# Optimization experiments

Measured on AMD Instinct MI355X. Metric: run time of the kernel, lower is better.

Reference implementation:

```python
import jax, jax.numpy as jnp
import numpy as np

B, NQ, NM, NHR, D, H, FF = 16, 100, 5440, 4096, 256, 8, 2048

def _ln(x, w, b):
    m = x.mean(-1, keepdims=True)
    v = ((x - m) ** 2).mean(-1, keepdims=True)
    return (x - m) * jax.lax.rsqrt(v + 1e-5) * w + b

def setup_inputs():
    key = jax.random.key(0)
    ks = iter(jax.random.split(key, 32))
    def rn(shape, s=1.0):
        return jax.random.normal(next(ks), shape, jnp.float32) * s
    return {
        'tgt': rn((B, NQ, D)),
        'memory': rn((B, NM, D)),
        'memory_hr': rn((B, NHR, D)),
        'prior_attn_bias': rn((B, NQ, NM)),
        'query_pos': rn((B, NQ, D)),
        'ln_cross_w': jnp.ones((D,)), 'ln_cross_b': jnp.zeros((D,)),
        'q_w': rn((D, D), 0.02), 'q_b': jnp.zeros((D,)),
        'k_w': rn((D, D), 0.02), 'k_b': jnp.zeros((D,)),
        'v_w': rn((D, D), 0.02), 'v_b': jnp.zeros((D,)),
        'out_w': rn((D, D), 0.02), 'out_b': jnp.zeros((D,)),
        'ln_self_w': jnp.ones((D,)), 'ln_self_b': jnp.zeros((D,)),
        'sa_in_w': rn((3 * D, D), 0.02), 'sa_in_b': jnp.zeros((3 * D,)),
        'sa_out_w': rn((D, D), 0.02), 'sa_out_b': jnp.zeros((D,)),
        'ln_ffn_w': jnp.ones((D,)), 'ln_ffn_b': jnp.zeros((D,)),
        'lin1_w': rn((FF, D), 0.02), 'lin1_b': jnp.zeros((FF,)),
        'lin2_w': rn((D, FF), 0.02), 'lin2_b': jnp.zeros((D,)),
        'me_w': rn((D, D), 0.02), 'me_b': jnp.zeros((D,)),
    }

def reference(tgt, memory, memory_hr, prior_attn_bias, query_pos,
              ln_cross_w, ln_cross_b, q_w, q_b, k_w, k_b, v_w, v_b,
              out_w, out_b, ln_self_w, ln_self_b, sa_in_w, sa_in_b,
              sa_out_w, sa_out_b, ln_ffn_w, ln_ffn_b, lin1_w, lin1_b,
              lin2_w, lin2_b, me_w, me_b):
    b, nq, d = tgt.shape
    nm = memory.shape[1]
    h = H
    dh = d // h
    scale = dh ** -0.5
    # ---- cross-attention with additive prior bias (eval mode: dropout = id) ----
    x = _ln(tgt, ln_cross_w, ln_cross_b)
    q = ((x + query_pos) @ q_w.T + q_b).reshape(b, nq, h, dh)
    k = (memory @ k_w.T + k_b).reshape(b, nm, h, dh)
    v = (memory @ v_w.T + v_b).reshape(b, nm, h, dh)
    attn = jnp.einsum('bqhd,bmhd->bhqm', q, k) * scale + prior_attn_bias[:, None]  # [b,h,nq,nm]
    a = jax.nn.softmax(attn, axis=-1)
    o = jnp.einsum('bhqm,bmhd->bqhd', a, v).reshape(b, nq, d)
    tgt = tgt + (o @ out_w.T + out_b)
    # ---- self-attention (torch nn.MultiheadAttention, batch_first, eval) ----
    z = _ln(tgt, ln_self_w, ln_self_b)
    zq = z + query_pos
    qs = (zq @ sa_in_w[:d].T + sa_in_b[:d]).reshape(b, nq, h, dh)
    ks = (zq @ sa_in_w[d:2 * d].T + sa_in_b[d:2 * d]).reshape(b, nq, h, dh)
    vs = (z @ sa_in_w[2 * d:].T + sa_in_b[2 * d:]).reshape(b, nq, h, dh)
    sattn = jax.nn.softmax(jnp.einsum('bqhd,bmhd->bhqm', qs, ks) * scale, axis=-1)
    so = jnp.einsum('bhqm,bmhd->bqhd', sattn, vs).reshape(b, nq, d)
    tgt = tgt + (so @ sa_out_w.T + sa_out_b)
    # ---- FFN ----
    y = _ln(tgt, ln_ffn_w, ln_ffn_b)
    y = jax.nn.gelu(y @ lin1_w.T + lin1_b, approximate=False) @ lin2_w.T + lin2_b
    tgt = tgt + y
    # ---- mask branch ----
    mask_logits = jnp.einsum('bqd,bmd->bqm', tgt @ me_w.T + me_b, memory_hr)
    return (tgt, mask_logits)
```

## Files before the change

kernel.cpp:

```cpp
#include <hip/hip_runtime.h>

typedef unsigned short u16;
typedef unsigned int u32;
typedef __bf16 bf16x8 __attribute__((ext_vector_type(8)));
typedef float f32x4 __attribute__((ext_vector_type(4)));

__device__ __forceinline__ u16 f2b(float f) {
  u32 u = __float_as_uint(f);
  u32 r = (u + 0x7fffu + ((u >> 16) & 1u)) >> 16;
  return (u16)r;
}
__device__ __forceinline__ float b2f(u16 h) {
  return __uint_as_float(((u32)h) << 16);
}
__device__ __forceinline__ bf16x8 zero8() {
  union { uint4 u; bf16x8 v; } z; z.u = make_uint4(0u, 0u, 0u, 0u); return z.v;
}
__device__ __forceinline__ u32 cvtpk(float lo, float hi) {
  u32 r;
  asm("v_cvt_pk_bf16_f32 %0, %1, %2" : "=v"(r) : "v"(lo), "v"(hi));
  return r;
}

struct Seg { const float* in; u16* out; int n4; };
struct Segs { Seg s[9]; };

__global__ __launch_bounds__(256)
void f2b_multi_kernel(Segs segs) {
  const Seg sg = segs.s[blockIdx.y];
  const int i = blockIdx.x * 256 + threadIdx.x;
  if (i < sg.n4) {
    const float4 f = *(const float4*)(sg.in + (size_t)i * 4);
    uint2 pk;
    pk.x = (u32)f2b(f.x) | ((u32)f2b(f.y) << 16);
    pk.y = (u32)f2b(f.z) | ((u32)f2b(f.w) << 16);
    *(uint2*)(sg.out + (size_t)i * 4) = pk;
  }
}

__global__ void copy_bias_kernel(const float* __restrict__ a, const float* __restrict__ b,
                                 float* __restrict__ out) {
  int i = threadIdx.x;
  out[i] = (i < 256) ? a[i] : b[i - 256];
}

__global__ __launch_bounds__(256)
void bias_tr_kernel(const float* __restrict__ bias, u16* __restrict__ biasT)
{
  __shared__ float S[100][69];
  const int tid = threadIdx.x;
  const int m0 = blockIdx.x * 64, b = blockIdx.y;
  for (int idx = tid; idx < 1600; idx += 256) {
    const int q = idx >> 4, seg = idx & 15;
    const float4 v = *(const float4*)(bias + (size_t)(b * 100 + q) * 5440 + m0 + seg * 4);
    S[q][seg * 4 + 0] = v.x; S[q][seg * 4 + 1] = v.y;
    S[q][seg * 4 + 2] = v.z; S[q][seg * 4 + 3] = v.w;
  }
  __syncthreads();
  for (int idx = tid; idx < 1792; idx += 256) {
    const int m = idx / 28, qg = (idx % 28) * 4;
    u16 h[4];
#pragma unroll
    for (int r = 0; r < 4; ++r) {
      const int q = qg + r;
      h[r] = (q < 100) ? f2b(S[q][m]) : (u16)0;
    }
    uint2 pk;
    pk.x = (u32)h[0] | ((u32)h[1] << 16);
    pk.y = (u32)h[2] | ((u32)h[3] << 16);
    *(uint2*)(biasT + ((size_t)(b * 5440 + m0 + m)) * 112 + qg) = pk;
  }
}

__global__ __launch_bounds__(256)
void ln_kernel(const float* __restrict__ x, const float* __restrict__ w, const float* __restrict__ b,
               const float* __restrict__ pos, u16* __restrict__ outz, u16* __restrict__ outzq)
{
  const int lane = threadIdx.x & 63;
  const int row = blockIdx.x * 4 + (threadIdx.x >> 6);
  const size_t o = (size_t)row * 256 + lane * 4;
  const float4 v = *(const float4*)(x + o);
  float s = v.x + v.y + v.z + v.w;
#pragma unroll
  for (int m = 1; m < 64; m <<= 1) s += __shfl_xor(s, m);
  const float mean = s * (1.f / 256.f);
  const float d0 = v.x - mean, d1 = v.y - mean, d2 = v.z - mean, d3 = v.w - mean;
  float ss = d0 * d0 + d1 * d1 + d2 * d2 + d3 * d3;
#pragma unroll
  for (int m = 1; m < 64; m <<= 1) ss += __shfl_xor(ss, m);
  const float rs = rsqrtf(ss * (1.f / 256.f) + 1e-5f);
  const float4 wv = *(const float4*)(w + lane * 4);
  const float4 bv = *(const float4*)(b + lane * 4);
  float y0 = d0 * rs * wv.x + bv.x;
  float y1 = d1 * rs * wv.y + bv.y;
  float y2 = d2 * rs * wv.z + bv.z;
  float y3 = d3 * rs * wv.w + bv.w;
  if (outz) {
    uint2 pk;
    pk.x = (u32)f2b(y0) | ((u32)f2b(y1) << 16);
    pk.y = (u32)f2b(y2) | ((u32)f2b(y3) << 16);
    *(uint2*)(outz + o) = pk;
  }
  if (outzq) {
    const float4 pv = *(const float4*)(pos + o);
    uint2 pk;
    pk.x = (u32)f2b(y0 + pv.x) | ((u32)f2b(y1 + pv.y) << 16);
    pk.y = (u32)f2b(y2 + pv.z) | ((u32)f2b(y3 + pv.w) << 16);
    *(uint2*)(outzq + o) = pk;
  }
}

template<int BM, int BN, int WM, int WN, int AF32, int GELU_, int RES_, int OF32, int OBF>
__global__ __launch_bounds__(256)
void gemm_kernel(const void* __restrict__ Ap, const u16* __restrict__ W,
                 const float* __restrict__ bias, const float* __restrict__ res,
                 float* __restrict__ Cf, u16* __restrict__ Cb,
                 int M, int N, int K, float scale)
{
  constexpr int WROWS = BM / WM;
  constexpr int WCOLS = BN / WN;
  constexpr int MT = WROWS / 16;
  constexpr int NT = WCOLS / 16;
  static_assert(WM * WN == 4, "4 waves");
  __shared__ u16 As[BM][40];
  __shared__ u16 Ws[BN][40];
  const int tid = threadIdx.x, lane = tid & 63, wid = tid >> 6;
  const int g = lane >> 4, lr = lane & 15;
  const int m0 = blockIdx.x * BM, n0 = blockIdx.y * BN;
  const int wm = wid / WN, wn = wid % WN;
  f32x4 acc[MT][NT] = {};
  for (int k0 = 0; k0 < K; k0 += 32) {
    for (int cid = tid; cid < BM * 4; cid += 256) {
      int r = cid >> 2, cg = (cid & 3) * 8;
      if constexpr (AF32) {
        const float* ap = (const float*)Ap + (size_t)(m0 + r) * K + k0 + cg;
        float4 f0 = *(const float4*)ap;
        float4 f1 = *(const float4*)(ap + 4);
        uint4 pk;
        pk.x = (u32)f2b(f0.x) | ((u32)f2b(f0.y) << 16);
        pk.y = (u32)f2b(f0.z) | ((u32)f2b(f0.w) << 16);
        pk.z = (u32)f2b(f1.x) | ((u32)f2b(f1.y) << 16);
        pk.w = (u32)f2b(f1.z) | ((u32)f2b(f1.w) << 16);
        *(uint4*)&As[r][cg] = pk;
      } else {
        *(uint4*)&As[r][cg] = *(const uint4*)((const u16*)Ap + (size_t)(m0 + r) * K + k0 + cg);
      }
    }
    for (int cid = tid; cid < BN * 4; cid += 256) {
      int r = cid >> 2, cg = (cid & 3) * 8;
      *(uint4*)&Ws[r][cg] = *(const uint4*)(W + (size_t)(n0 + r) * K + k0 + cg);
    }
    __syncthreads();
    bf16x8 af[MT], bfr[NT];
#pragma unroll
    for (int mt = 0; mt < MT; ++mt) af[mt] = *(const bf16x8*)&As[wm * WROWS + mt * 16 + lr][g * 8];
#pragma unroll
    for (int nt = 0; nt < NT; ++nt) bfr[nt] = *(const bf16x8*)&Ws[wn * WCOLS + nt * 16 + lr][g * 8];
#pragma unroll
    for (int mt = 0; mt < MT; ++mt)
#pragma unroll
      for (int nt = 0; nt < NT; ++nt)
        acc[mt][nt] = __builtin_amdgcn_mfma_f32_16x16x32_bf16(af[mt], bfr[nt], acc[mt][nt], 0, 0, 0);
    __syncthreads();
  }
#pragma unroll
  for (int mt = 0; mt < MT; ++mt)
#pragma unroll
    for (int nt = 0; nt < NT; ++nt) {
      const int col = n0 + wn * WCOLS + nt * 16 + lr;
      const float bv = bias[col];
#pragma unroll
      for (int r = 0; r < 4; ++r) {
        const int row = m0 + wm * WROWS + mt * 16 + g * 4 + r;
        float v = (acc[mt][nt][r] + bv) * scale;
        if constexpr (GELU_) v = 0.5f * v * (1.f + erff(v * 0.70710678118654752f));
        if constexpr (RES_) v += res[(size_t)row * N + col];
        if constexpr (OF32) Cf[(size_t)row * N + col] = v;
        if constexpr (OBF) Cb[(size_t)row * N + col] = f2b(v);
      }
    }
}

__global__ __launch_bounds__(512, 4)
void kv_gemm_kernel(const float* __restrict__ A, const u16* __restrict__ Wk,
                    const u16* __restrict__ Wv, const float* __restrict__ biasKV,
                    u16* __restrict__ Kb, u16* __restrict__ Vt)
{
  __shared__ u16 As[64 * 256];
  const int tid = threadIdx.x, lane = tid & 63, wid = tid >> 6;
  const int g = lane >> 4, lr = lane & 15;
  const int bidx = blockIdx.x / 85, t = blockIdx.x - bidx * 85;
  const int row0 = blockIdx.x * 64;

  for (int ch = tid; ch < 2048; ch += 512) {
    const int r = ch >> 5, c8 = (ch & 31) * 8;
    const float* ap = A + (size_t)(row0 + r) * 256 + c8;
    const float4 f0 = *(const float4*)ap;
    const float4 f1 = *(const float4*)(ap + 4);
    uint4 pk;
    pk.x = cvtpk(f0.x, f0.y);
    pk.y = cvtpk(f0.z, f0.w);
    pk.z = cvtpk(f1.x, f1.y);
    pk.w = cvtpk(f1.z, f1.w);
    const int byte = r * 512 + c8 * 2;
    *(uint4*)((char*)As + (byte ^ ((r & 7) << 4))) = pk;
  }
  __syncthreads();

  const int isV = wid >> 2;
  const u16* W = isV ? Wv : Wk;
  const int n0 = (wid & 3) * 64;
  const u16* Wb[4];
#pragma unroll
  for (int nt = 0; nt < 4; ++nt)
    Wb[nt] = W + (size_t)(n0 + nt * 16 + lr) * 256 + g * 8;

  f32x4 acc[4][4] = {};
#pragma unroll 2
  for (int ks = 0; ks < 8; ++ks) {
    bf16x8 bfv[4], af[4];
#pragma unroll
    for (int nt = 0; nt < 4; ++nt)
      bfv[nt] = *(const bf16x8*)(Wb[nt] + ks * 32);
#pragma unroll
    for (int mt = 0; mt < 4; ++mt) {
      const int r = mt * 16 + lr;
      const int byte = r * 512 + ks * 64 + g * 16;
      af[mt] = *(const bf16x8*)((const char*)As + (byte ^ ((r & 7) << 4)));
    }
#pragma unroll
    for (int mt = 0; mt < 4; ++mt)
#pragma unroll
      for (int nt = 0; nt < 4; ++nt)
        acc[mt][nt] = __builtin_amdgcn_mfma_f32_16x16x32_bf16(af[mt], bfv[nt], acc[mt][nt], 0, 0, 0);
  }

  if (!isV) {
#pragma unroll
    for (int nt = 0; nt < 4; ++nt) {
      const int col = n0 + nt * 16 + lr;
      const float bv = biasKV[col];
#pragma unroll
      for (int mt = 0; mt < 4; ++mt)
#pragma unroll
        for (int r = 0; r < 4; ++r)
          Kb[(size_t)(row0 + mt * 16 + g * 4 + r) * 256 + col] = f2b(acc[mt][nt][r] + bv);
    }
  } else {
    const int mloc0 = t * 64;
#pragma unroll
    for (int nt = 0; nt < 4; ++nt) {
      const int col = n0 + nt * 16 + lr;
      const float bv = biasKV[256 + col];
      const size_t rowbase = ((size_t)(bidx * 8 + (col >> 5)) * 32 + (col & 31)) * 5440;
#pragma unroll
      for (int mt = 0; mt < 4; ++mt)
#pragma unroll
        for (int r = 0; r < 4; ++r) {
          const int mloc = mloc0 + mt * 16 + g * 4 + r;
          const int ml = mloc & 31;
          const int p = 8 * ((ml & 15) >> 2) + 2 * (ml & 3) + (ml >> 4);
          Vt[rowbase + (mloc & ~31) + p] = f2b(acc[mt][nt][r] + bv);
        }
    }
  }
}

__global__ __launch_bounds__(256, 3)
void cross_attn_kernel(const u16* __restrict__ Q, const u16* __restrict__ Kb,
                       const u16* __restrict__ Vt, const u16* __restrict__ biasT,
                       float* __restrict__ Opart, float* __restrict__ ML)
{
  __shared__ u32 P32[4][112][20];
  const int tid = threadIdx.x, lane = tid & 63, wid = tid >> 6;
  const int g = lane >> 4, lr = lane & 15;
  const int b = blockIdx.y, c = blockIdx.x;
  const int head = blockIdx.z * 4 + wid;
  const int m_base = c * 320;
  const f32x4 zf = {0.f, 0.f, 0.f, 0.f};

  bf16x8 qf[7];
#pragma unroll
  for (int mt = 0; mt < 7; ++mt) {
    int qr = mt * 16 + lr;
    qf[mt] = (qr < 100) ? *(const bf16x8*)&Q[(size_t)(b * 100 + qr) * 256 + head * 32 + g * 8]
                        : zero8();
  }
  float Mst[7];
  f32x4 Lp[7];
  f32x4 Oa[7][2];
#pragma unroll
  for (int mt = 0; mt < 7; ++mt) { Mst[mt] = -1e30f; Lp[mt] = zf; Oa[mt][0] = zf; Oa[mt][1] = zf; }

  for (int s = 0; s < 10; ++s) {
    const int m0 = m_base + s * 32;
    const bf16x8 kf0 = *(const bf16x8*)&Kb[(size_t)(b * 5440 + m0 + lr) * 256 + head * 32 + g * 8];
    const bf16x8 kf1 = *(const bf16x8*)&Kb[(size_t)(b * 5440 + m0 + 16 + lr) * 256 + head * 32 + g * 8];
    const size_t vrow = ((size_t)(b * 8 + head) * 32 + lr) * 5440 + m0 + g * 8;
    const bf16x8 vf0 = *(const bf16x8*)&Vt[vrow];
    const bf16x8 vf1 = *(const bf16x8*)&Vt[vrow + 16 * 5440];
    const u16* bb = biasT + ((size_t)(b * 5440 + m0 + lr)) * 112 + g * 4;
#pragma unroll
    for (int mt = 0; mt < 7; ++mt) {
      f32x4 s0 = __builtin_amdgcn_mfma_f32_16x16x32_bf16(qf[mt], kf0, zf, 0, 0, 0);
      f32x4 s1 = __builtin_amdgcn_mfma_f32_16x16x32_bf16(qf[mt], kf1, zf, 0, 0, 0);
      const uint2 b0 = *(const uint2*)(bb + mt * 16);
      const uint2 b1 = *(const uint2*)(bb + 16 * 112 + mt * 16);
      s0[0] += b2f((u16)b0.x);      s0[1] += b2f((u16)(b0.x >> 16));
      s0[2] += b2f((u16)b0.y);      s0[3] += b2f((u16)(b0.y >> 16));
      s1[0] += b2f((u16)b1.x);      s1[1] += b2f((u16)(b1.x >> 16));
      s1[2] += b2f((u16)b1.y);      s1[3] += b2f((u16)(b1.y >> 16));
      float mx = fmaxf(fmaxf(fmaxf(s0[0], s0[1]), fmaxf(s0[2], s0[3])),
                       fmaxf(fmaxf(s1[0], s1[1]), fmaxf(s1[2], s1[3])));
#pragma unroll
      for (int d = 1; d < 16; d <<= 1) mx = fmaxf(mx, __shfl_xor(mx, d, 16));
      const float newM = fmaxf(Mst[mt], mx);
      const float al = __expf(Mst[mt] - newM);
      Mst[mt] = newM;
      f32x4 p0, p1;
#pragma unroll
      for (int r = 0; r < 4; ++r) {
        p0[r] = __expf(s0[r] - newM);
        p1[r] = __expf(s1[r] - newM);
      }
      Lp[mt] = Lp[mt] * al + (p0 + p1);
      Oa[mt][0] *= al;
      Oa[mt][1] *= al;
#pragma unroll
      for (int r = 0; r < 4; ++r)
        P32[wid][mt * 16 + g * 4 + r][lr] = (u32)f2b(p0[r]) | ((u32)f2b(p1[r]) << 16);
    }
#pragma unroll
    for (int mt = 0; mt < 7; ++mt) {
      const bf16x8 pa = *(const bf16x8*)&P32[wid][mt * 16 + lr][g * 4];
      Oa[mt][0] = __builtin_amdgcn_mfma_f32_16x16x32_bf16(pa, vf0, Oa[mt][0], 0, 0, 0);
      Oa[mt][1] = __builtin_amdgcn_mfma_f32_16x16x32_bf16(pa, vf1, Oa[mt][1], 0, 0, 0);
    }
  }
  const int bh = b * 8 + head;
#pragma unroll
  for (int mt = 0; mt < 7; ++mt)
#pragma unroll
    for (int r = 0; r < 4; ++r) {
      const int qr = mt * 16 + g * 4 + r;
      if (qr < 100) {
        float L = Lp[mt][r];
#pragma unroll
        for (int d = 1; d < 16; d <<= 1) L += __shfl_xor(L, d, 16);
        const size_t rb = (size_t)(bh * 17 + c) * 100 + qr;
        Opart[rb * 32 + lr] = Oa[mt][0][r];
        Opart[rb * 32 + 16 + lr] = Oa[mt][1][r];
        if (lr == 0) { ML[rb * 2] = Mst[mt]; ML[rb * 2 + 1] = L; }
      }
    }
}

__global__ __launch_bounds__(256)
void reduce_attn_kernel(const float* __restrict__ Opart, const float* __restrict__ ML,
                        u16* __restrict__ outb)
{
  const int row = blockIdx.x;
  const int b = row / 100, q = row % 100;
  const int h = threadIdx.x >> 5, d = threadIdx.x & 31;
  const int bh = b * 8 + h;
  float gm = -1e30f;
  for (int c = 0; c < 17; ++c) gm = fmaxf(gm, ML[((size_t)(bh * 17 + c) * 100 + q) * 2]);
  float l = 0.f, o = 0.f;
  for (int c = 0; c < 17; ++c) {
    const size_t rb = (size_t)(bh * 17 + c) * 100 + q;
    const float w = __expf(ML[rb * 2] - gm);
    l += ML[rb * 2 + 1] * w;
    o += Opart[rb * 32 + d] * w;
  }
  outb[(size_t)row * 256 + h * 32 + d] = f2b(o / l);
}

__global__ __launch_bounds__(128)
void self_attn_kernel(const float* __restrict__ qk, const float* __restrict__ vs,
                      u16* __restrict__ so)
{
  __shared__ u16 kk[100][36];
  __shared__ u16 vv[100][36];
  __shared__ float S[100][101];
  const int b = blockIdx.x >> 3, h = blockIdx.x & 7;
  const int t = threadIdx.x;
  for (int e = t; e < 3200; e += 128) {
    const int r = e >> 5, cq = e & 31;
    kk[r][cq] = f2b(qk[(size_t)(b * 100 + r) * 512 + 256 + h * 32 + cq]);
    vv[r][cq] = f2b(vs[(size_t)(b * 100 + r) * 256 + h * 32 + cq]);
  }
  __syncthreads();
  if (t < 100) {
    float qr_[32];
#pragma unroll
    for (int cq = 0; cq < 32; ++cq) qr_[cq] = qk[(size_t)(b * 100 + t) * 512 + h * 32 + cq];
    for (int m = 0; m < 100; ++m) {
      float dp = 0.f;
#pragma unroll
      for (int cq = 0; cq < 32; ++cq) dp += qr_[cq] * b2f(kk[m][cq]);
      S[t][m] = dp * 0.17677669529663687f;
    }
    float mx = -1e30f;
    for (int m = 0; m < 100; ++m) mx = fmaxf(mx, S[t][m]);
    float sum = 0.f;
    for (int m = 0; m < 100; ++m) { const float p = __expf(S[t][m] - mx); S[t][m] = p; sum += p; }
    const float inv = 1.f / sum;
    float o[32];
#pragma unroll
    for (int cq = 0; cq < 32; ++cq) o[cq] = 0.f;
    for (int m = 0; m < 100; ++m) {
      const float p = S[t][m];
#pragma unroll
      for (int cq = 0; cq < 32; ++cq) o[cq] += p * b2f(vv[m][cq]);
    }
#pragma unroll
    for (int cq = 0; cq < 32; ++cq)
      so[(size_t)(b * 100 + t) * 256 + h * 32 + cq] = f2b(o[cq] * inv);
  }
}

__global__ __launch_bounds__(256)
void mask_gemm_kernel(const u16* __restrict__ tm, const float* __restrict__ hr,
                      float* __restrict__ out)
{
  __shared__ u16 As[112][40];
  __shared__ u16 Bs[64][40];
  const int tid = threadIdx.x, lane = tid & 63, wid = tid >> 6;
  const int g = lane >> 4, lr = lane & 15;
  const int b = blockIdx.y, n0 = blockIdx.x * 64;
  f32x4 acc[7] = {};
  for (int k0 = 0; k0 < 256; k0 += 32) {
    for (int cid = tid; cid < 448; cid += 256) {
      const int r = cid >> 2, cg = (cid & 3) * 8;
      uint4 val = {0u, 0u, 0u, 0u};
      if (r < 100) val = *(const uint4*)&tm[(size_t)(b * 100 + r) * 256 + k0 + cg];
      *(uint4*)&As[r][cg] = val;
    }
    {
      const int r = tid >> 2, cg = (tid & 3) * 8;
      const float* hp = hr + (size_t)(b * 4096 + n0 + r) * 256 + k0 + cg;
      float4 f0 = *(const float4*)hp;
      float4 f1 = *(const float4*)(hp + 4);
      uint4 pk;
      pk.x = (u32)f2b(f0.x) | ((u32)f2b(f0.y) << 16);
      pk.y = (u32)f2b(f0.z) | ((u32)f2b(f0.w) << 16);
      pk.z = (u32)f2b(f1.x) | ((u32)f2b(f1.y) << 16);
      pk.w = (u32)f2b(f1.z) | ((u32)f2b(f1.w) << 16);
      *(uint4*)&Bs[r][cg] = pk;
    }
    __syncthreads();
    const bf16x8 bfr = *(const bf16x8*)&Bs[wid * 16 + lr][g * 8];
#pragma unroll
    for (int mt = 0; mt < 7; ++mt) {
      const bf16x8 af = *(const bf16x8*)&As[mt * 16 + lr][g * 8];
      acc[mt] = __builtin_amdgcn_mfma_f32_16x16x32_bf16(af, bfr, acc[mt], 0, 0, 0);
    }
    __syncthreads();
  }
#pragma unroll
  for (int mt = 0; mt < 7; ++mt)
#pragma unroll
    for (int r = 0; r < 4; ++r) {
      const int qr = mt * 16 + g * 4 + r;
      if (qr < 100)
        out[(size_t)(b * 100 + qr) * 4096 + n0 + wid * 16 + lr] = acc[mt][r];
    }
}

extern "C" void kernel_launch(void* const* d_in, const int* in_sizes, int n_in,
                              void* d_out, int out_size, void* d_ws, size_t ws_size,
                              hipStream_t stream)
{
  (void)in_sizes; (void)n_in; (void)out_size; (void)ws_size;
  const float* tgt      = (const float*)d_in[0];
  const float* memory   = (const float*)d_in[1];
  const float* memhr    = (const float*)d_in[2];
  const float* pbias    = (const float*)d_in[3];
  const float* qpos     = (const float*)d_in[4];
  const float* lncw     = (const float*)d_in[5];
  const float* lncb     = (const float*)d_in[6];
  const float* q_w      = (const float*)d_in[7];
  const float* q_b      = (const float*)d_in[8];
  const float* k_w      = (const float*)d_in[9];
  const float* k_b      = (const float*)d_in[10];
  const float* v_w      = (const float*)d_in[11];
  const float* v_b      = (const float*)d_in[12];
  const float* out_w    = (const float*)d_in[13];
  const float* out_b    = (const float*)d_in[14];
  const float* lnsw     = (const float*)d_in[15];
  const float* lnsb     = (const float*)d_in[16];
  const float* sa_in_w  = (const float*)d_in[17];
  const float* sa_in_b  = (const float*)d_in[18];
  const float* sa_out_w = (const float*)d_in[19];
  const float* sa_out_b = (const float*)d_in[20];
  const float* lnfw     = (const float*)d_in[21];
  const float* lnfb     = (const float*)d_in[22];
  const float* l1w      = (const float*)d_in[23];
  const float* l1b      = (const float*)d_in[24];
  const float* l2w      = (const float*)d_in[25];
  const float* l2b      = (const float*)d_in[26];
  const float* me_w     = (const float*)d_in[27];
  const float* me_b     = (const float*)d_in[28];
  float* outf = (float*)d_out;

  char* ws = (char*)d_ws;
  size_t off = 0;
  auto alloc = [&](size_t bytes) -> void* {
    void* p = ws + off;
    off = (off + bytes + 255) & ~(size_t)255;
    return p;
  };
  u16*   kvW   = (u16*)alloc((size_t)131072 * 2);
  u16*   qW    = (u16*)alloc((size_t)65536 * 2);
  u16*   outW  = (u16*)alloc((size_t)65536 * 2);
  u16*   saW   = (u16*)alloc((size_t)196608 * 2);
  u16*   saoW  = (u16*)alloc((size_t)65536 * 2);
  u16*   l1W   = (u16*)alloc((size_t)524288 * 2);
  u16*   l2W   = (u16*)alloc((size_t)524288 * 2);
  u16*   meW   = (u16*)alloc((size_t)65536 * 2);
  float* kvB   = (float*)alloc((size_t)512 * 4);
  u16*   biasT = (u16*)alloc((size_t)9748480 * 2);
  u16*   zq1   = (u16*)alloc((size_t)409600 * 2);
  u16*   Qb    = (u16*)alloc((size_t)409600 * 2);
  u16*   Kb    = (u16*)alloc((size_t)22282240 * 2);
  u16*   Vt    = (u16*)alloc((size_t)22282240 * 2);
  float* Opart = (float*)alloc((size_t)6963200 * 4);
  float* MLp   = (float*)alloc((size_t)435200 * 4);
  u16*   attno = (u16*)alloc((size_t)409600 * 2);
  float* tgt1  = (float*)alloc((size_t)409600 * 4);
  u16*   z2    = (u16*)alloc((size_t)409600 * 2);
  u16*   zq2   = (u16*)alloc((size_t)409600 * 2);
  float* qkb   = (float*)alloc((size_t)819200 * 4);
  float* vsb   = (float*)alloc((size_t)409600 * 4);
  u16*   sob   = (u16*)alloc((size_t)409600 * 2);
  float* tgt2  = (float*)alloc((size_t)409600 * 4);
  u16*   y0b   = (u16*)alloc((size_t)409600 * 2);
  u16*   hb    = (u16*)alloc((size_t)3276800 * 2);
  u16*   t3b   = (u16*)alloc((size_t)409600 * 2);
  u16*   tmb   = (u16*)alloc((size_t)409600 * 2);

  const float SCALE = 0.17677669529663687f;

  Segs segs;
  segs.s[0] = {k_w,      kvW,          16384};
  segs.s[1] = {v_w,      kvW + 65536,  16384};
  segs.s[2] = {q_w,      qW,           16384};
  segs.s[3] = {out_w,    outW,         16384};
  segs.s[4] = {sa_in_w,  saW,          49152};
  segs.s[5] = {sa_out_w, saoW,         16384};
  segs.s[6] = {l1w,      l1W,          131072};
  segs.s[7] = {l2w,      l2W,          131072};
  segs.s[8] = {me_w,     meW,          16384};
  f2b_multi_kernel<<<dim3(512, 9), 256, 0, stream>>>(segs);
  copy_bias_kernel<<<1, 512, 0, stream>>>(k_b, v_b, kvB);
  bias_tr_kernel<<<dim3(85, 16), 256, 0, stream>>>(pbias, biasT);

  ln_kernel<<<400, 256, 0, stream>>>(tgt, lncw, lncb, qpos, nullptr, zq1);
  gemm_kernel<16, 128, 1, 4, 0, 0, 0, 0, 1><<<dim3(100, 2), 256, 0, stream>>>(
      zq1, qW, q_b, nullptr, nullptr, Qb, 1600, 256, 256, SCALE);
  kv_gemm_kernel<<<dim3(1360), 512, 0, stream>>>(memory, kvW, kvW + 65536, kvB, Kb, Vt);
  cross_attn_kernel<<<dim3(17, 16, 2), 256, 0, stream>>>(Qb, Kb, Vt, biasT, Opart, MLp);
  reduce_attn_kernel<<<1600, 256, 0, stream>>>(Opart, MLp, attno);
  gemm_kernel<16, 128, 1, 4, 0, 0, 1, 1, 0><<<dim3(100, 2), 256, 0, stream>>>(
      attno, outW, out_b, tgt, tgt1, nullptr, 1600, 256, 256, 1.f);

  ln_kernel<<<400, 256, 0, stream>>>(tgt1, lnsw, lnsb, qpos, z2, zq2);
  gemm_kernel<16, 128, 1, 4, 0, 0, 0, 1, 0><<<dim3(100, 4), 256, 0, stream>>>(
      zq2, saW, sa_in_b, nullptr, qkb, nullptr, 1600, 512, 256, 1.f);
  gemm_kernel<16, 128, 1, 4, 0, 0, 0, 1, 0><<<dim3(100, 2), 256, 0, stream>>>(
      z2, saW + 131072, sa_in_b + 512, nullptr, vsb, nullptr, 1600, 256, 256, 1.f);
  self_attn_kernel<<<128, 128, 0, stream>>>(qkb, vsb, sob);
  gemm_kernel<16, 128, 1, 4, 0, 0, 1, 1, 0><<<dim3(100, 2), 256, 0, stream>>>(
      sob, saoW, sa_out_b, tgt1, tgt2, nullptr, 1600, 256, 256, 1.f);

  ln_kernel<<<400, 256, 0, stream>>>(tgt2, lnfw, lnfb, nullptr, y0b, nullptr);
  gemm_kernel<64, 256, 4, 1, 0, 1, 0, 0, 1><<<dim3(25, 8), 256, 0, stream>>>(
      y0b, l1W, l1b, nullptr, nullptr, hb, 1600, 2048, 256, 1.f);
  gemm_kernel<16, 128, 1, 4, 0, 0, 1, 1, 1><<<dim3(100, 2), 256, 0, stream>>>(
      hb, l2W, l2b, tgt2, outf, t3b, 1600, 256, 2048, 1.f);

  gemm_kernel<16, 128, 1, 4, 0, 0, 0, 0, 1><<<dim3(100, 2), 256, 0, stream>>>(
      t3b, meW, me_b, nullptr, nullptr, tmb, 1600, 256, 256, 1.f);
  mask_gemm_kernel<<<dim3(64, 16), 256, 0, stream>>>(tmb, memhr, outf + 409600);
}
```

Baseline: 370.7 us.

## Fuse prep kernels, fold layernorms into GEMMs, restage KV epilogue via LDS

```diff
diff --git a/kernel.cpp b/kernel.cpp
--- a/kernel.cpp
+++ b/kernel.cpp
@@ -23,96 +23,231 @@
 }
 
 struct Seg { const float* in; u16* out; int n4; };
-struct Segs { Seg s[9]; };
+struct PrepArgs {
+  Seg seg[7];
+  const float *k_w, *v_w, *k_b, *v_b, *pbias;
+  u16 *Wf, *biasT;
+  float *kvB;
+};
 
 __global__ __launch_bounds__(256)
-void f2b_multi_kernel(Segs segs) {
-  const Seg sg = segs.s[blockIdx.y];
-  const int i = blockIdx.x * 256 + threadIdx.x;
-  if (i < sg.n4) {
-    const float4 f = *(const float4*)(sg.in + (size_t)i * 4);
-    uint2 pk;
-    pk.x = (u32)f2b(f.x) | ((u32)f2b(f.y) << 16);
-    pk.y = (u32)f2b(f.z) | ((u32)f2b(f.w) << 16);
-    *(uint2*)(sg.out + (size_t)i * 4) = pk;
-  }
-}
-
-__global__ void copy_bias_kernel(const float* __restrict__ a, const float* __restrict__ b,
-                                 float* __restrict__ out) {
-  int i = threadIdx.x;
-  out[i] = (i < 256) ? a[i] : b[i - 256];
-}
-
-__global__ __launch_bounds__(256)
-void bias_tr_kernel(const float* __restrict__ bias, u16* __restrict__ biasT)
+void prep_kernel(PrepArgs a)
 {
   __shared__ float S[100][69];
-  const int tid = threadIdx.x;
-  const int m0 = blockIdx.x * 64, b = blockIdx.y;
-  for (int idx = tid; idx < 1600; idx += 256) {
-    const int q = idx >> 4, seg = idx & 15;
-    const float4 v = *(const float4*)(bias + (size_t)(b * 100 + q) * 5440 + m0 + seg * 4);
-    S[q][seg * 4 + 0] = v.x; S[q][seg * 4 + 1] = v.y;
-    S[q][seg * 4 + 2] = v.z; S[q][seg * 4 + 3] = v.w;
-  }
-  __syncthreads();
-  for (int idx = tid; idx < 1792; idx += 256) {
-    const int m = idx / 28, qg = (idx % 28) * 4;
-    u16 h[4];
-#pragma unroll
-    for (int r = 0; r < 4; ++r) {
-      const int q = qg + r;
-      h[r] = (q < 100) ? f2b(S[q][m]) : (u16)0;
-    }
-    uint2 pk;
-    pk.x = (u32)h[0] | ((u32)h[1] << 16);
-    pk.y = (u32)h[2] | ((u32)h[3] << 16);
-    *(uint2*)(biasT + ((size_t)(b * 5440 + m0 + m)) * 112 + qg) = pk;
-  }
-}
-
-__global__ __launch_bounds__(256)
-void ln_kernel(const float* __restrict__ x, const float* __restrict__ w, const float* __restrict__ b,
-               const float* __restrict__ pos, u16* __restrict__ outz, u16* __restrict__ outzq)
-{
-  const int lane = threadIdx.x & 63;
-  const int row = blockIdx.x * 4 + (threadIdx.x >> 6);
-  const size_t o = (size_t)row * 256 + lane * 4;
-  const float4 v = *(const float4*)(x + o);
-  float s = v.x + v.y + v.z + v.w;
-#pragma unroll
-  for (int m = 1; m < 64; m <<= 1) s += __shfl_xor(s, m);
-  const float mean = s * (1.f / 256.f);
-  const float d0 = v.x - mean, d1 = v.y - mean, d2 = v.z - mean, d3 = v.w - mean;
-  float ss = d0 * d0 + d1 * d1 + d2 * d2 + d3 * d3;
-#pragma unroll
-  for (int m = 1; m < 64; m <<= 1) ss += __shfl_xor(ss, m);
-  const float rs = rsqrtf(ss * (1.f / 256.f) + 1e-5f);
+  const int bx = blockIdx.x, tid = threadIdx.x;
+  if (bx < 1472) {
+    int bxr = bx;
+#pragma unroll
+    for (int k = 0; k < 7; ++k) {
+      const int nb = a.seg[k].n4 >> 8;
+      if (bxr < nb) {
+        const int i = bxr * 256 + tid;
+        const float4 f = *(const float4*)(a.seg[k].in + (size_t)i * 4);
+        uint2 pk; pk.x = cvtpk(f.x, f.y); pk.y = cvtpk(f.z, f.w);
+        *(uint2*)(a.seg[k].out + (size_t)i * 4) = pk;
+        return;
+      }
+      bxr -= nb;
+    }
+    return;
+  } else if (bx < 1536) {
+    const int i = bx - 1472, gI = i >> 3, ks = i & 7;
+    const int nt = tid >> 6, lane = tid & 63, lr = lane & 15, g = lane >> 4;
+    const float* src = (gI < 4 ? a.k_w + (size_t)(gI * 64 + nt * 16 + lr) * 256
+                               : a.v_w + (size_t)((gI - 4) * 64 + nt * 16 + lr) * 256)
+                       + ks * 32 + g * 8;
+    const float4 f0 = *(const float4*)src;
+    const float4 f1 = *(const float4*)(src + 4);
+    uint4 pk;
+    pk.x = cvtpk(f0.x, f0.y); pk.y = cvtpk(f0.z, f0.w);
+    pk.z = cvtpk(f1.x, f1.y); pk.w = cvtpk(f1.z, f1.w);
+    *(uint4*)(a.Wf + (size_t)((gI * 8 + ks) * 4 + nt) * 512 + lane * 8) = pk;
+  } else if (bx < 1538) {
+    const int i = (bx - 1536) * 256 + tid;
+    a.kvB[i] = (i < 256) ? a.k_b[i] : a.v_b[i - 256];
+  } else {
+    const int bt = bx - 1538;
+    const int b = bt / 85, m0 = (bt - b * 85) * 64;
+    for (int idx = tid; idx < 1600; idx += 256) {
+      const int q = idx >> 4, seg = idx & 15;
+      const float4 v = *(const float4*)(a.pbias + (size_t)(b * 100 + q) * 5440 + m0 + seg * 4);
+      S[q][seg * 4 + 0] = v.x; S[q][seg * 4 + 1] = v.y;
+      S[q][seg * 4 + 2] = v.z; S[q][seg * 4 + 3] = v.w;
+    }
+    __syncthreads();
+    for (int idx = tid; idx < 1792; idx += 256) {
+      const int m = idx / 28, qg = (idx % 28) * 4;
+      u16 h[4];
+#pragma unroll
+      for (int r = 0; r < 4; ++r) {
+        const int q = qg + r;
+        h[r] = (q < 100) ? f2b(S[q][m]) : (u16)0;
+      }
+      uint2 pk;
+      pk.x = (u32)h[0] | ((u32)h[1] << 16);
+      pk.y = (u32)h[2] | ((u32)h[3] << 16);
+      *(uint2*)(a.biasT + ((size_t)(b * 5440 + m0 + m)) * 112 + qg) = pk;
+    }
+  }
+}
+
+template<int ROWS>
+__device__ __forceinline__ void ln_stage(const float* __restrict__ x, int row0,
+    const float* __restrict__ w, const float* __restrict__ b,
+    const float* __restrict__ pos, u16* As)
+{
+  const int tid = threadIdx.x, lane = tid & 63, wid = tid >> 6;
   const float4 wv = *(const float4*)(w + lane * 4);
   const float4 bv = *(const float4*)(b + lane * 4);
-  float y0 = d0 * rs * wv.x + bv.x;
-  float y1 = d1 * rs * wv.y + bv.y;
-  float y2 = d2 * rs * wv.z + bv.z;
-  float y3 = d3 * rs * wv.w + bv.w;
-  if (outz) {
-    uint2 pk;
-    pk.x = (u32)f2b(y0) | ((u32)f2b(y1) << 16);
-    pk.y = (u32)f2b(y2) | ((u32)f2b(y3) << 16);
-    *(uint2*)(outz + o) = pk;
-  }
-  if (outzq) {
-    const float4 pv = *(const float4*)(pos + o);
-    uint2 pk;
-    pk.x = (u32)f2b(y0 + pv.x) | ((u32)f2b(y1 + pv.y) << 16);
-    pk.y = (u32)f2b(y2 + pv.z) | ((u32)f2b(y3 + pv.w) << 16);
-    *(uint2*)(outzq + o) = pk;
-  }
-}
-
-template<int BM, int BN, int WM, int WN, int AF32, int GELU_, int RES_, int OF32, int OBF>
+#pragma unroll
+  for (int rr = 0; rr < ROWS / 4; ++rr) {
+    const int rl = wid * (ROWS / 4) + rr;
+    const size_t o = (size_t)(row0 + rl) * 256 + lane * 4;
+    const float4 v = *(const float4*)(x + o);
+    float s = v.x + v.y + v.z + v.w;
+#pragma unroll
+    for (int m = 1; m < 64; m <<= 1) s += __shfl_xor(s, m);
+    const float mean = s * (1.f / 256.f);
+    const float d0 = v.x - mean, d1 = v.y - mean, d2 = v.z - mean, d3 = v.w - mean;
+    float ss = d0 * d0 + d1 * d1 + d2 * d2 + d3 * d3;
+#pragma unroll
+    for (int m = 1; m < 64; m <<= 1) ss += __shfl_xor(ss, m);
+    const float rs = rsqrtf(ss * (1.f / 256.f) + 1e-5f);
+    float y0 = d0 * rs * wv.x + bv.x;
+    float y1 = d1 * rs * wv.y + bv.y;
+    float y2 = d2 * rs * wv.z + bv.z;
+    float y3 = d3 * rs * wv.w + bv.w;
+    if (pos) {
+      const float4 pv = *(const float4*)(pos + o);
+      y0 += pv.x; y1 += pv.y; y2 += pv.z; y3 += pv.w;
+    }
+    uint2 pk; pk.x = cvtpk(y0, y1); pk.y = cvtpk(y2, y3);
+    const int byte = (rl * 512 + lane * 8) ^ ((rl & 7) << 4);
+    *(uint2*)((char*)As + byte) = pk;
+  }
+}
+
+__device__ __forceinline__ void gemm16x128(const u16* As, const u16* __restrict__ W,
+                                           u16 (*Ws)[40], f32x4 acc[2])
+{
+  const int tid = threadIdx.x, lane = tid & 63, wid = tid >> 6;
+  const int g = lane >> 4, lr = lane & 15;
+  for (int k0 = 0; k0 < 256; k0 += 32) {
+    for (int cid = tid; cid < 512; cid += 256) {
+      const int r = cid >> 2, cg = (cid & 3) * 8;
+      *(uint4*)&Ws[r][cg] = *(const uint4*)(W + (size_t)r * 256 + k0 + cg);
+    }
+    __syncthreads();
+    const int abyte = (lr * 512 + k0 * 2 + g * 16) ^ ((lr & 7) << 4);
+    const bf16x8 af = *(const bf16x8*)((const char*)As + abyte);
+#pragma unroll
+    for (int nt = 0; nt < 2; ++nt) {
+      const bf16x8 bfr = *(const bf16x8*)&Ws[wid * 32 + nt * 16 + lr][g * 8];
+      acc[nt] = __builtin_amdgcn_mfma_f32_16x16x32_bf16(af, bfr, acc[nt], 0, 0, 0);
+    }
+    __syncthreads();
+  }
+}
+
 __global__ __launch_bounds__(256)
-void gemm_kernel(const void* __restrict__ Ap, const u16* __restrict__ W,
+void qproj_kernel(const float* __restrict__ x, const float* __restrict__ lnw,
+                  const float* __restrict__ lnb, const float* __restrict__ pos,
+                  const u16* __restrict__ W, const float* __restrict__ bias,
+                  u16* __restrict__ out, float scale)
+{
+  __shared__ u16 As[16 * 256];
+  __shared__ u16 Ws[128][40];
+  const int tid = threadIdx.x, lane = tid & 63, wid = tid >> 6;
+  const int g = lane >> 4, lr = lane & 15;
+  const int row0 = blockIdx.x * 16, n0 = blockIdx.y * 128;
+  ln_stage<16>(x, row0, lnw, lnb, pos, As);
+  f32x4 acc[2] = {};
+  gemm16x128(As, W + (size_t)n0 * 256, Ws, acc);
+#pragma unroll
+  for (int nt = 0; nt < 2; ++nt) {
+    const int col = n0 + wid * 32 + nt * 16 + lr;
+    const float bv = bias[col];
+#pragma unroll
+    for (int r = 0; r < 4; ++r) {
+      const int row = row0 + g * 4 + r;
+      out[(size_t)row * 256 + col] = f2b((acc[nt][r] + bv) * scale);
+    }
+  }
+}
+
+__global__ __launch_bounds__(256)
+void sain_kernel(const float* __restrict__ x, const float* __restrict__ lnw,
+                 const float* __restrict__ lnb, const float* __restrict__ pos,
+                 const u16* __restrict__ W, const float* __restrict__ bias,
+                 float* __restrict__ qkb, float* __restrict__ vsb)
+{
+  __shared__ u16 As[16 * 256];
+  __shared__ u16 Ws[128][40];
+  const int tid = threadIdx.x, lane = tid & 63, wid = tid >> 6;
+  const int g = lane >> 4, lr = lane & 15;
+  const int row0 = blockIdx.x * 16, y = blockIdx.y;
+  ln_stage<16>(x, row0, lnw, lnb, (y < 4) ? pos : nullptr, As);
+  f32x4 acc[2] = {};
+  gemm16x128(As, W + (size_t)y * 128 * 256, Ws, acc);
+#pragma unroll
+  for (int nt = 0; nt < 2; ++nt) {
+    const int cl = wid * 32 + nt * 16 + lr;
+    const float bv = bias[y * 128 + cl];
+#pragma unroll
+    for (int r = 0; r < 4; ++r) {
+      const int row = row0 + g * 4 + r;
+      const float v = acc[nt][r] + bv;
+      if (y < 4) qkb[(size_t)row * 512 + y * 128 + cl] = v;
+      else       vsb[(size_t)row * 256 + (y - 4) * 128 + cl] = v;
+    }
+  }
+}
+
+__global__ __launch_bounds__(256)
+void ffn1_kernel(const float* __restrict__ x, const float* __restrict__ lnw,
+                 const float* __restrict__ lnb, const u16* __restrict__ W,
+                 const float* __restrict__ bias, u16* __restrict__ out)
+{
+  __shared__ u16 As[64 * 256];
+  __shared__ u16 Ws[256][40];
+  const int tid = threadIdx.x, lane = tid & 63, wid = tid >> 6;
+  const int g = lane >> 4, lr = lane & 15;
+  const int row0 = blockIdx.x * 64, n0 = blockIdx.y * 256;
+  ln_stage<64>(x, row0, lnw, lnb, nullptr, As);
+  f32x4 acc[16] = {};
+  for (int k0 = 0; k0 < 256; k0 += 32) {
+    for (int cid = tid; cid < 1024; cid += 256) {
+      const int r = cid >> 2, cg = (cid & 3) * 8;
+      *(uint4*)&Ws[r][cg] = *(const uint4*)(W + (size_t)(n0 + r) * 256 + k0 + cg);
+    }
+    __syncthreads();
+    const int arow = wid * 16 + lr;
+    const int abyte = (arow * 512 + k0 * 2 + g * 16) ^ ((arow & 7) << 4);
+    const bf16x8 af = *(const bf16x8*)((const char*)As + abyte);
+#pragma unroll
+    for (int nt = 0; nt < 16; ++nt) {
+      const bf16x8 bfr = *(const bf16x8*)&Ws[nt * 16 + lr][g * 8];
+      acc[nt] = __builtin_amdgcn_mfma_f32_16x16x32_bf16(af, bfr, acc[nt], 0, 0, 0);
+    }
+    __syncthreads();
+  }
+#pragma unroll
+  for (int nt = 0; nt < 16; ++nt) {
+    const int col = n0 + nt * 16 + lr;
+    const float bv = bias[col];
+#pragma unroll
+    for (int r = 0; r < 4; ++r) {
+      const int row = row0 + wid * 16 + g * 4 + r;
+      float v = acc[nt][r] + bv;
+      v = 0.5f * v * (1.f + erff(v * 0.70710678118654752f));
+      out[(size_t)row * 2048 + col] = f2b(v);
+    }
+  }
+}
+
+template<int BM, int BN, int WM, int WN, int GELU_, int RES_, int OF32, int OBF>
+__global__ __launch_bounds__(256)
+void gemm_kernel(const u16* __restrict__ Ap, const u16* __restrict__ W,
                  const float* __restrict__ bias, const float* __restrict__ res,
                  float* __restrict__ Cf, u16* __restrict__ Cb,
                  int M, int N, int K, float scale)
@@ -132,19 +267,7 @@
   for (int k0 = 0; k0 < K; k0 += 32) {
     for (int cid = tid; cid < BM * 4; cid += 256) {
       int r = cid >> 2, cg = (cid & 3) * 8;
-      if constexpr (AF32) {
-        const float* ap = (const float*)Ap + (size_t)(m0 + r) * K + k0 + cg;
-        float4 f0 = *(const float4*)ap;
-        float4 f1 = *(const float4*)(ap + 4);
-        uint4 pk;
-        pk.x = (u32)f2b(f0.x) | ((u32)f2b(f0.y) << 16);
-        pk.y = (u32)f2b(f0.z) | ((u32)f2b(f0.w) << 16);
-        pk.z = (u32)f2b(f1.x) | ((u32)f2b(f1.y) << 16);
-        pk.w = (u32)f2b(f1.z) | ((u32)f2b(f1.w) << 16);
-        *(uint4*)&As[r][cg] = pk;
-      } else {
-        *(uint4*)&As[r][cg] = *(const uint4*)((const u16*)Ap + (size_t)(m0 + r) * K + k0 + cg);
-      }
+      *(uint4*)&As[r][cg] = *(const uint4*)(Ap + (size_t)(m0 + r) * K + k0 + cg);
     }
     for (int cid = tid; cid < BN * 4; cid += 256) {
       int r = cid >> 2, cg = (cid & 3) * 8;
@@ -182,8 +305,8 @@
 }
 
 __global__ __launch_bounds__(512, 4)
-void kv_gemm_kernel(const float* __restrict__ A, const u16* __restrict__ Wk,
-                    const u16* __restrict__ Wv, const float* __restrict__ biasKV,
+void kv_gemm_kernel(const float* __restrict__ A, const u16* __restrict__ Wf,
+                    const float* __restrict__ biasKV,
                     u16* __restrict__ Kb, u16* __restrict__ Vt)
 {
   __shared__ u16 As[64 * 256];
@@ -207,21 +330,14 @@
   }
   __syncthreads();
 
-  const int isV = wid >> 2;
-  const u16* W = isV ? Wv : Wk;
-  const int n0 = (wid & 3) * 64;
-  const u16* Wb[4];
-#pragma unroll
-  for (int nt = 0; nt < 4; ++nt)
-    Wb[nt] = W + (size_t)(n0 + nt * 16 + lr) * 256 + g * 8;
-
+  const u16* wbase = Wf + (size_t)wid * 8 * 4 * 512 + lane * 8;
   f32x4 acc[4][4] = {};
 #pragma unroll 2
   for (int ks = 0; ks < 8; ++ks) {
     bf16x8 bfv[4], af[4];
 #pragma unroll
     for (int nt = 0; nt < 4; ++nt)
-      bfv[nt] = *(const bf16x8*)(Wb[nt] + ks * 32);
+      bfv[nt] = *(const bf16x8*)(wbase + (ks * 4 + nt) * 512);
 #pragma unroll
     for (int mt = 0; mt < 4; ++mt) {
       const int r = mt * 16 + lr;
@@ -234,35 +350,60 @@
       for (int nt = 0; nt < 4; ++nt)
         acc[mt][nt] = __builtin_amdgcn_mfma_f32_16x16x32_bf16(af[mt], bfv[nt], acc[mt][nt], 0, 0, 0);
   }
-
+  __syncthreads();
+
+  const int isV = wid >> 2;
+  if (isV) {
+#pragma unroll
+    for (int nt = 0; nt < 4; ++nt) {
+      const int col = (wid - 4) * 64 + nt * 16 + lr;
+      const float bv = biasKV[256 + col];
+#pragma unroll
+      for (int mt = 0; mt < 4; ++mt)
+#pragma unroll
+        for (int r = 0; r < 4; ++r) {
+          const int slot = (mt >> 1) * 32 + 8 * g + 2 * r + (mt & 1);
+          const int byte = (col * 128 + slot * 2) ^ ((col & 7) << 4);
+          *(u16*)((char*)As + byte) = f2b(acc[mt][nt][r] + bv);
+        }
+    }
+  }
+  __syncthreads();
+  {
+    const size_t vbase = (size_t)bidx * 256 * 5440 + (size_t)t * 64;
+#pragma unroll
+    for (int p = 0; p < 4; ++p) {
+      const int idx = p * 512 + tid;
+      const int col = idx >> 3, chunk = idx & 7;
+      const int lbyte = col * 128 + ((chunk * 16) ^ ((col & 7) << 4));
+      const uint4 v = *(const uint4*)((const char*)As + lbyte);
+      *(uint4*)(Vt + vbase + (size_t)col * 5440 + chunk * 8) = v;
+    }
+  }
+  __syncthreads();
   if (!isV) {
 #pragma unroll
     for (int nt = 0; nt < 4; ++nt) {
-      const int col = n0 + nt * 16 + lr;
+      const int col = wid * 64 + nt * 16 + lr;
       const float bv = biasKV[col];
 #pragma unroll
       for (int mt = 0; mt < 4; ++mt)
 #pragma unroll
-        for (int r = 0; r < 4; ++r)
-          Kb[(size_t)(row0 + mt * 16 + g * 4 + r) * 256 + col] = f2b(acc[mt][nt][r] + bv);
-    }
-  } else {
-    const int mloc0 = t * 64;
-#pragma unroll
-    for (int nt = 0; nt < 4; ++nt) {
-      const int col = n0 + nt * 16 + lr;
-      const float bv = biasKV[256 + col];
-      const size_t rowbase = ((size_t)(bidx * 8 + (col >> 5)) * 32 + (col & 31)) * 5440;
-#pragma unroll
-      for (int mt = 0; mt < 4; ++mt)
-#pragma unroll
         for (int r = 0; r < 4; ++r) {
-          const int mloc = mloc0 + mt * 16 + g * 4 + r;
-          const int ml = mloc & 31;
-          const int p = 8 * ((ml & 15) >> 2) + 2 * (ml & 3) + (ml >> 4);
-          Vt[rowbase + (mloc & ~31) + p] = f2b(acc[mt][nt][r] + bv);
+          const int row = mt * 16 + g * 4 + r;
+          const int byte = (row * 512 + col * 2) ^ ((row & 7) << 4);
+          *(u16*)((char*)As + byte) = f2b(acc[mt][nt][r] + bv);
         }
     }
+  }
+  __syncthreads();
+#pragma unroll
+  for (int p = 0; p < 4; ++p) {
+    const int idx = p * 512 + tid;
+    const int row = idx >> 5, c16 = idx & 31;
+    const int lbyte = row * 512 + ((c16 * 16) ^ ((row & 7) << 4));
+    const uint4 v = *(const uint4*)((const char*)As + lbyte);
+    *(uint4*)(Kb + (size_t)(row0 + row) * 256 + c16 * 8) = v;
   }
 }
 
@@ -442,10 +583,8 @@
       float4 f0 = *(const float4*)hp;
       float4 f1 = *(const float4*)(hp + 4);
       uint4 pk;
-      pk.x = (u32)f2b(f0.x) | ((u32)f2b(f0.y) << 16);
-      pk.y = (u32)f2b(f0.z) | ((u32)f2b(f0.w) << 16);
-      pk.z = (u32)f2b(f1.x) | ((u32)f2b(f1.y) << 16);
-      pk.w = (u32)f2b(f1.z) | ((u32)f2b(f1.w) << 16);
+      pk.x = cvtpk(f0.x, f0.y); pk.y = cvtpk(f0.z, f0.w);
+      pk.z = cvtpk(f1.x, f1.y); pk.w = cvtpk(f1.z, f1.w);
       *(uint4*)&Bs[r][cg] = pk;
     }
     __syncthreads();
@@ -510,7 +649,7 @@
     off = (off + bytes + 255) & ~(size_t)255;
     return p;
   };
-  u16*   kvW   = (u16*)alloc((size_t)131072 * 2);
+  u16*   Wf    = (u16*)alloc((size_t)131072 * 2);
   u16*   qW    = (u16*)alloc((size_t)65536 * 2);
   u16*   outW  = (u16*)alloc((size_t)65536 * 2);
   u16*   saW   = (u16*)alloc((size_t)196608 * 2);
@@ -520,7 +659,6 @@
   u16*   meW   = (u16*)alloc((size_t)65536 * 2);
   float* kvB   = (float*)alloc((size_t)512 * 4);
   u16*   biasT = (u16*)alloc((size_t)9748480 * 2);
-  u16*   zq1   = (u16*)alloc((size_t)409600 * 2);
   u16*   Qb    = (u16*)alloc((size_t)409600 * 2);
   u16*   Kb    = (u16*)alloc((size_t)22282240 * 2);
   u16*   Vt    = (u16*)alloc((size_t)22282240 * 2);
@@ -528,58 +666,45 @@
   float* MLp   = (float*)alloc((size_t)435200 * 4);
   u16*   attno = (u16*)alloc((size_t)409600 * 2);
   float* tgt1  = (float*)alloc((size_t)409600 * 4);
-  u16*   z2    = (u16*)alloc((size_t)409600 * 2);
-  u16*   zq2   = (u16*)alloc((size_t)409600 * 2);
   float* qkb   = (float*)alloc((size_t)819200 * 4);
   float* vsb   = (float*)alloc((size_t)409600 * 4);
   u16*   sob   = (u16*)alloc((size_t)409600 * 2);
   float* tgt2  = (float*)alloc((size_t)409600 * 4);
-  u16*   y0b   = (u16*)alloc((size_t)409600 * 2);
   u16*   hb    = (u16*)alloc((size_t)3276800 * 2);
   u16*   t3b   = (u16*)alloc((size_t)409600 * 2);
   u16*   tmb   = (u16*)alloc((size_t)409600 * 2);
 
   const float SCALE = 0.17677669529663687f;
 
-  Segs segs;
-  segs.s[0] = {k_w,      kvW,          16384};
-  segs.s[1] = {v_w,      kvW + 65536,  16384};
-  segs.s[2] = {q_w,      qW,           16384};
-  segs.s[3] = {out_w,    outW,         16384};
-  segs.s[4] = {sa_in_w,  saW,          49152};
-  segs.s[5] = {sa_out_w, saoW,         16384};
-  segs.s[6] = {l1w,      l1W,          131072};
-  segs.s[7] = {l2w,      l2W,          131072};
-  segs.s[8] = {me_w,     meW,          16384};
-  f2b_multi_kernel<<<dim3(512, 9), 256, 0, stream>>>(segs);
-  copy_bias_kernel<<<1, 512, 0, stream>>>(k_b, v_b, kvB);
-  bias_tr_kernel<<<dim3(85, 16), 256, 0, stream>>>(pbias, biasT);
-
-  ln_kernel<<<400, 256, 0, stream>>>(tgt, lncw, lncb, qpos, nullptr, zq1);
-  gemm_kernel<16, 128, 1, 4, 0, 0, 0, 0, 1><<<dim3(100, 2), 256, 0, stream>>>(
-      zq1, qW, q_b, nullptr, nullptr, Qb, 1600, 256, 256, SCALE);
-  kv_gemm_kernel<<<dim3(1360), 512, 0, stream>>>(memory, kvW, kvW + 65536, kvB, Kb, Vt);
+  PrepArgs pa;
+  pa.seg[0] = {q_w,      qW,   16384};
+  pa.seg[1] = {out_w,    outW, 16384};
+  pa.seg[2] = {sa_in_w,  saW,  49152};
+  pa.seg[3] = {sa_out_w, saoW, 16384};
+  pa.seg[4] = {l1w,      l1W,  131072};
+  pa.seg[5] = {l2w,      l2W,  131072};
+  pa.seg[6] = {me_w,     meW,  16384};
+  pa.k_w = k_w; pa.v_w = v_w; pa.k_b = k_b; pa.v_b = v_b; pa.pbias = pbias;
+  pa.Wf = Wf; pa.biasT = biasT; pa.kvB = kvB;
+  prep_kernel<<<2898, 256, 0, stream>>>(pa);
+
+  qproj_kernel<<<dim3(100, 2), 256, 0, stream>>>(tgt, lncw, lncb, qpos, qW, q_b, Qb, SCALE);
+  kv_gemm_kernel<<<dim3(1360), 512, 0, stream>>>(memory, Wf, kvB, Kb, Vt);
   cross_attn_kernel<<<dim3(17, 16, 2), 256, 0, stream>>>(Qb, Kb, Vt, biasT, Opart, MLp);
   reduce_attn_kernel<<<1600, 256, 0, stream>>>(Opart, MLp, attno);
-  gemm_kernel<16, 128, 1, 4, 0, 0, 1, 1, 0><<<dim3(100, 2), 256, 0, stream>>>(
+  gemm_kernel<16, 128, 1, 4, 0, 1, 1, 0><<<dim3(100, 2), 256, 0, stream>>>(
       attno, outW, out_b, tgt, tgt1, nullptr, 1600, 256, 256, 1.f);
 
-  ln_kernel<<<400, 256, 0, stream>>>(tgt1, lnsw, lnsb, qpos, z2, zq2);
-  gemm_kernel<16, 128, 1, 4, 0, 0, 0, 1, 0><<<dim3(100, 4), 256, 0, stream>>>(
-      zq2, saW, sa_in_b, nullptr, qkb, nullptr, 1600, 512, 256, 1.f);
-  gemm_kernel<16, 128, 1, 4, 0, 0, 0, 1, 0><<<dim3(100, 2), 256, 0, stream>>>(
-      z2, saW + 131072, sa_in_b + 512, nullptr, vsb, nullptr, 1600, 256, 256, 1.f);
+  sain_kernel<<<dim3(100, 6), 256, 0, stream>>>(tgt1, lnsw, lnsb, qpos, saW, sa_in_b, qkb, vsb);
   self_attn_kernel<<<128, 128, 0, stream>>>(qkb, vsb, sob);
-  gemm_kernel<16, 128, 1, 4, 0, 0, 1, 1, 0><<<dim3(100, 2), 256, 0, stream>>>(
+  gemm_kernel<16, 128, 1, 4, 0, 1, 1, 0><<<dim3(100, 2), 256, 0, stream>>>(
       sob, saoW, sa_out_b, tgt1, tgt2, nullptr, 1600, 256, 256, 1.f);
 
-  ln_kernel<<<400, 256, 0, stream>>>(tgt2, lnfw, lnfb, nullptr, y0b, nullptr);
-  gemm_kernel<64, 256, 4, 1, 0, 1, 0, 0, 1><<<dim3(25, 8), 256, 0, stream>>>(
-      y0b, l1W, l1b, nullptr, nullptr, hb, 1600, 2048, 256, 1.f);
-  gemm_kernel<16, 128, 1, 4, 0, 0, 1, 1, 1><<<dim3(100, 2), 256, 0, stream>>>(
+  ffn1_kernel<<<dim3(25, 8), 256, 0, stream>>>(tgt2, lnfw, lnfb, l1W, l1b, hb);
+  gemm_kernel<16, 128, 1, 4, 0, 1, 1, 1><<<dim3(100, 2), 256, 0, stream>>>(
       hb, l2W, l2b, tgt2, outf, t3b, 1600, 256, 2048, 1.f);
 
-  gemm_kernel<16, 128, 1, 4, 0, 0, 0, 0, 1><<<dim3(100, 2), 256, 0, stream>>>(
+  gemm_kernel<16, 128, 1, 4, 0, 0, 0, 1><<<dim3(100, 2), 256, 0, stream>>>(
       t3b, meW, me_b, nullptr, nullptr, tmb, 1600, 256, 256, 1.f);
   mask_gemm_kernel<<<dim3(64, 16), 256, 0, stream>>>(tmb, memhr, outf + 409600);
 }
```

Measured after the change: 339.5 us. -8.4%, faster.
